# Kernel optimization log

Measured on AMD Instinct MI355X. Metric: run time of the kernel, lower is better.

Reference implementation:

```python
import jax, jax.numpy as jnp
import numpy as np
import string

N_QUBITS = 16
N_LAYERS = 2
BATCH = 32
DIM = 2 ** N_QUBITS


def _apply_1q(psi, U, q):
    # psi: (B,) + (2,)*n complex; U: (2,2) complex acting on qubit q
    n = psi.ndim - 1
    ax = string.ascii_lowercase[:n]
    out = list(ax)
    out[q] = 'A'
    return jnp.einsum('A' + ax[q] + ',z' + ax + '->z' + ''.join(out), U, psi)


def _apply_2q(psi, G, c, t):
    # G: (2,2,2,2) = (out_c, out_t, in_c, in_t)
    n = psi.ndim - 1
    ax = string.ascii_lowercase[:n]
    out = list(ax)
    out[c] = 'A'
    out[t] = 'B'
    return jnp.einsum('AB' + ax[c] + ax[t] + ',z' + ax + '->z' + ''.join(out), G, psi)


def _rx(th):
    c = jnp.cos(th * 0.5).astype(jnp.complex64)
    s = jnp.sin(th * 0.5).astype(jnp.complex64)
    return jnp.array([[c, -1j * s], [-1j * s, c]])


def _ry(th):
    c = jnp.cos(th * 0.5).astype(jnp.complex64)
    s = jnp.sin(th * 0.5).astype(jnp.complex64)
    return jnp.array([[c, -s], [s, c]])


def _rz(th):
    th_c = th.astype(jnp.complex64)
    z = jnp.zeros((), jnp.complex64)
    return jnp.array([[jnp.exp(-0.5j * th_c), z], [z, jnp.exp(0.5j * th_c)]])


_CNOT = jnp.array([[1, 0, 0, 0],
                   [0, 1, 0, 0],
                   [0, 0, 0, 1],
                   [0, 0, 1, 0]], dtype=jnp.complex64).reshape(2, 2, 2, 2)


def setup_inputs() -> dict:
    key = jax.random.key(0)
    k1, k2, k3 = jax.random.split(key, 3)
    thetas = jax.random.normal(k1, (N_LAYERS, 3, N_QUBITS), dtype=jnp.float32)
    re = jax.random.normal(k2, (BATCH, DIM), dtype=jnp.float32)
    im = jax.random.normal(k3, (BATCH, DIM), dtype=jnp.float32)
    norm = jnp.sqrt(jnp.sum(re * re + im * im, axis=-1, keepdims=True))
    return {"thetas": thetas, "state_re": re / norm, "state_im": im / norm}


def reference(thetas, state_re, state_im):
    B = state_re.shape[0]
    psi = (state_re.astype(jnp.complex64) + 1j * state_im.astype(jnp.complex64))
    psi = psi.reshape((B,) + (2,) * N_QUBITS)
    for l in range(N_LAYERS):
        for q in range(N_QUBITS):
            psi = _apply_1q(psi, _rx(thetas[l, 0, q]), q)
            psi = _apply_1q(psi, _ry(thetas[l, 1, q]), q)
            psi = _apply_1q(psi, _rz(thetas[l, 2, q]), q)
        for q in range(N_QUBITS):
            psi = _apply_2q(psi, _CNOT, q, (q + 1) % N_QUBITS)
    probs = (psi.real ** 2 + psi.imag ** 2).reshape(B, -1)
    return probs
```

## Files before the change

### kernel.cpp

```cpp
#include <hip/hip_runtime.h>


#define NT 256

__device__ __forceinline__ int fperm(int x) {
  int y = x ^ (x >> 1);
  y ^= (x & 1) ? 0xC000 : 0;
  return y & 0xFFFF;
}

__device__ __forceinline__ int finv16(int x) {
  int s = x;
  s ^= s >> 1; s ^= s >> 2; s ^= s >> 4; s ^= s >> 8;
  int b15 = ((s ^ (s >> 15)) & 1) << 15;
  return (s & 0x7FFF) | b15;
}

__device__ __forceinline__ int swz1(int l) { return l ^ ((l >> 4) & 31); }
__device__ __forceinline__ int swz2(int l) { return l ^ ((l >> 5) & 31); }

__device__ __forceinline__ void compute_gates(const float* __restrict__ th, float* gsh) {
  int tid = threadIdx.x;
  if (tid < 32) {
    int l = tid >> 4, q = tid & 15;
    float tx = th[l * 48 + q], ty = th[l * 48 + 16 + q], tz = th[l * 48 + 32 + q];
    float cx, sx, cy, sy, cz, sz;
    sincosf(0.5f * tx, &sx, &cx);
    sincosf(0.5f * ty, &sy, &cy);
    sincosf(0.5f * tz, &sz, &cz);
    float m00r = cy * cx, m00i =  sy * sx;
    float m01r = -sy * cx, m01i = -cy * sx;
    float m10r =  sy * cx, m10i = -cy * sx;
    float m11r =  cy * cx, m11i = -sy * sx;
    float* G = gsh + tid * 8;
    G[0] = cz * m00r + sz * m00i;  G[1] = cz * m00i - sz * m00r;
    G[2] = cz * m01r + sz * m01i;  G[3] = cz * m01i - sz * m01r;
    G[4] = cz * m10r - sz * m10i;  G[5] = cz * m10i + sz * m10r;
    G[6] = cz * m11r - sz * m11i;  G[7] = cz * m11i + sz * m11r;
  }
}

template <int MK, int SK, int N>
__device__ __forceinline__ void greg(float (&ar)[N], float (&ai)[N],
                                     const float* G, int c) {
  const float4* G4 = (const float4*)G;
  float4 r0 = G4[0], r1 = G4[1];
  bool sw = (c != 0);
  float h00r = sw ? r1.z : r0.x, h00i = sw ? r1.w : r0.y;
  float h01r = sw ? r1.x : r0.z, h01i = sw ? r1.y : r0.w;
  float h10r = sw ? r0.z : r1.x, h10i = sw ? r0.w : r1.y;
  float h11r = sw ? r0.x : r1.z, h11i = sw ? r0.y : r1.w;
  constexpr int PV = MK & (-MK);
#pragma unroll
  for (int k = 0; k < N; k++) {
    if (k & PV) continue;
    const int k2 = k ^ MK;
    const int p0 = __builtin_popcount(k & SK) & 1;
    const int ka = p0 ? k2 : k;
    const int kb = p0 ? k : k2;
    float xr = ar[ka], xi = ai[ka], yr = ar[kb], yi = ai[kb];
    ar[ka] = h00r * xr - h00i * xi + h01r * yr - h01i * yi;
    ai[ka] = h00r * xi + h00i * xr + h01r * yi + h01i * yr;
    ar[kb] = h10r * xr - h10i * xi + h11r * yr - h11i * yi;
    ai[kb] = h10r * xi + h10i * xr + h11r * yi + h11i * yr;
  }
}

__global__ void __launch_bounds__(NT) pass1_k(const float* __restrict__ th,
                                              const float* __restrict__ xre,
                                              const float* __restrict__ xim,
                                              float2* __restrict__ ws) {
  __shared__ float gsh[256];
  __shared__ float sre[4096], sim[4096];
  int t = threadIdx.x;
  int blk = blockIdx.x, batch = blk >> 4, wb = blk & 15;
  int base = batch * 65536 + (wb << 12);
  float ar[16], ai[16];

  compute_gates(th, gsh);
  {
    const float4* xr4 = (const float4*)(xre + base + (t << 4));
    const float4* xi4 = (const float4*)(xim + base + (t << 4));
#pragma unroll
    for (int q = 0; q < 4; q++) {
      float4 v = xr4[q]; ar[4*q] = v.x; ar[4*q+1] = v.y; ar[4*q+2] = v.z; ar[4*q+3] = v.w;
      float4 w = xi4[q]; ai[4*q] = w.x; ai[4*q+1] = w.y; ai[4*q+2] = w.z; ai[4*q+3] = w.w;
    }
  }
  __syncthreads();
  greg<1, 1>(ar, ai, gsh + 15 * 8, 0);
  greg<2, 2>(ar, ai, gsh + 14 * 8, 0);
  greg<4, 4>(ar, ai, gsh + 13 * 8, 0);
  greg<8, 8>(ar, ai, gsh + 12 * 8, 0);
#pragma unroll
  for (int k = 0; k < 16; k++) { int s = swz1((t << 4) | k); sre[s] = ar[k]; sim[s] = ai[k]; }
  __syncthreads();
#pragma unroll
  for (int k = 0; k < 16; k++) {
    int s = swz1((t & 15) | (k << 4) | ((t >> 4) << 8));
    ar[k] = sre[s]; ai[k] = sim[s];
  }
  greg<1, 1>(ar, ai, gsh + 11 * 8, 0);
  greg<2, 2>(ar, ai, gsh + 10 * 8, 0);
  greg<4, 4>(ar, ai, gsh + 9 * 8, 0);
  greg<8, 8>(ar, ai, gsh + 8 * 8, 0);
#pragma unroll
  for (int k = 0; k < 16; k++) {
    int s = swz1((t & 15) | (k << 4) | ((t >> 4) << 8));
    sre[s] = ar[k]; sim[s] = ai[k];
  }
  __syncthreads();
#pragma unroll
  for (int k = 0; k < 16; k++) {
    int s = swz1(t | (k << 8)); ar[k] = sre[s]; ai[k] = sim[s];
  }
  greg<1, 1>(ar, ai, gsh + 7 * 8, 0);
  greg<2, 2>(ar, ai, gsh + 6 * 8, 0);
  greg<4, 4>(ar, ai, gsh + 5 * 8, 0);
  greg<8, 8>(ar, ai, gsh + 4 * 8, 0);
#pragma unroll
  for (int k = 0; k < 16; k++)
    ws[base + t + (k << 8)] = make_float2(ar[k], ai[k]);
}

__global__ void __launch_bounds__(NT) pass2_k(const float* __restrict__ th,
                                              float2* __restrict__ ws) {
  __shared__ float gsh[256];
  __shared__ float sre[4096], sim[4096];
  int t = threadIdx.x;
  int blk = blockIdx.x, batch = blk >> 4, wb = blk & 15;
  int bbase = batch * 65536;
  float ar[16], ai[16];

  compute_gates(th, gsh);
#pragma unroll
  for (int k = 0; k < 16; k++) {
    float2 v = ws[bbase + t + (wb << 8) + (k << 12)];
    ar[k] = v.x; ai[k] = v.y;
  }
  __syncthreads();
  int cA = (__popc(t) + __popc(wb)) & 1;
  greg<1, 1>(ar, ai, gsh + 3 * 8, 0);
  greg<2, 2>(ar, ai, gsh + 2 * 8, 0);
  greg<4, 4>(ar, ai, gsh + 1 * 8, 0);
  greg<8, 8>(ar, ai, gsh + 0 * 8, 0);
  greg<12, 7>(ar, ai, gsh + (16 + 0) * 8, cA);
  greg<6, 12>(ar, ai, gsh + (16 + 1) * 8, 0);
  greg<3, 14>(ar, ai, gsh + (16 + 2) * 8, 0);
#pragma unroll
  for (int k = 0; k < 16; k++) {
    int s = swz2(t | (k << 8)); sre[s] = ar[k]; sim[s] = ai[k];
  }
  __syncthreads();
#pragma unroll
  for (int k = 0; k < 16; k++) {
    int s = swz2((k & 3) | (t << 2) | ((k >> 2) << 10));
    ar[k] = sre[s]; ai[k] = sim[s];
  }
  greg<13, 15>(ar, ai, gsh + (16 + 15) * 8, cA);
  greg<3, 14>(ar, ai, gsh + (16 + 14) * 8, cA);
#pragma unroll
  for (int k = 0; k < 16; k++) {
    int s = swz2((k & 3) | (t << 2) | ((k >> 2) << 10));
    sre[s] = ar[k]; sim[s] = ai[k];
  }
  __syncthreads();
#pragma unroll
  for (int k = 0; k < 16; k++) {
    int s = swz2((t & 1) | (k << 1) | ((t >> 1) << 5));
    ar[k] = sre[s]; ai[k] = sim[s];
  }
  {
    int cC = (__popc(t >> 1) + __popc(wb)) & 1;
    greg<3, 14>(ar, ai, gsh + (16 + 13) * 8, cC);
    greg<6, 12>(ar, ai, gsh + (16 + 12) * 8, cC);
    greg<12, 8>(ar, ai, gsh + (16 + 11) * 8, cC);
  }
#pragma unroll
  for (int k = 0; k < 16; k++) {
    int s = swz2((t & 1) | (k << 1) | ((t >> 1) << 5));
    sre[s] = ar[k]; sim[s] = ai[k];
  }
  __syncthreads();
#pragma unroll
  for (int k = 0; k < 16; k++) {
    int s = swz2((t & 15) | (k << 4) | ((t >> 4) << 8));
    ar[k] = sre[s]; ai[k] = sim[s];
  }
  {
    int cD = (__popc(t >> 4) + __popc(wb)) & 1;
    greg<3, 14>(ar, ai, gsh + (16 + 10) * 8, cD);
    greg<6, 12>(ar, ai, gsh + (16 + 9) * 8, cD);
    greg<12, 8>(ar, ai, gsh + (16 + 8) * 8, cD);
  }
#pragma unroll
  for (int k = 0; k < 16; k++) {
    int full = (t & 15) | (k << 4) | (wb << 8) | ((t >> 4) << 12);
    ws[bbase + full] = make_float2(ar[k], ai[k]);
  }
}

__global__ void __launch_bounds__(NT) pass3_k(const float* __restrict__ th,
                                              const float2* __restrict__ ws,
                                              float* __restrict__ out) {
  __shared__ float gsh[256];
  int t = threadIdx.x;
  int blk = blockIdx.x, batch = blk >> 3, g3 = blk & 7;
  int bbase = batch * 65536;
  int jt = t | (g3 << 13);
  float ar[32], ai[32];
  compute_gates(th, gsh);
#pragma unroll
  for (int k = 0; k < 32; k++) {
    int j = jt | (k << 8);
    float2 v = ws[bbase + fperm(j)];
    ar[k] = v.x; ai[k] = v.y;
  }
  __syncthreads();
  greg<1, 1>(ar, ai, gsh + (16 + 7) * 8, 0);
  greg<2, 2>(ar, ai, gsh + (16 + 6) * 8, 0);
  greg<4, 4>(ar, ai, gsh + (16 + 5) * 8, 0);
  greg<8, 8>(ar, ai, gsh + (16 + 4) * 8, 0);
  greg<16, 16>(ar, ai, gsh + (16 + 3) * 8, 0);
#pragma unroll
  for (int k = 0; k < 32; k++) {
    int j = jt | (k << 8);
    out[bbase + finv16(j)] = ar[k] * ar[k] + ai[k] * ai[k];
  }
}

extern "C" void kernel_launch(void* const* d_in, const int* in_sizes, int n_in,
                              void* d_out, int out_size, void* d_ws, size_t ws_size,
                              hipStream_t stream) {
  const float* th  = (const float*)d_in[0];
  const float* xre = (const float*)d_in[1];
  const float* xim = (const float*)d_in[2];
  float* out = (float*)d_out;

  float2* amp = (float2*)d_ws;

  pass1_k<<<512, NT, 0, stream>>>(th, xre, xim, amp);
  pass2_k<<<512, NT, 0, stream>>>(th, amp);
  pass3_k<<<256, NT, 0, stream>>>(th, amp, out);
}
```

Baseline: 104.2 us.

## Fuse three passes into one cooperative kernel with per-batch atomic counters

Merges the three separate kernel launches into a single cooperative kernel. The phases are synchronized per batch with global atomic counters and spin-waits instead of kernel boundaries, which lets batches progress independently and removes the launch gaps between passes. It adds a memset, an occupancy query and fence/atomic overhead on every call. It relies on co-residency of all 512 blocks and falls back to the three-kernel path if the cooperative launch fails.

```diff
diff --git a/kernel.cpp b/kernel.cpp
--- a/kernel.cpp
+++ b/kernel.cpp
@@ -66,6 +66,155 @@
   }
 }
 
+
+__device__ __forceinline__ void phaseA_body(int t, int bbase, int wb,
+                                            const float* gsh,
+                                            float* sre, float* sim,
+                                            const float* __restrict__ xre,
+                                            const float* __restrict__ xim,
+                                            float2* __restrict__ ws) {
+  float ar[16], ai[16];
+  int base = bbase + (wb << 12);
+  const float4* xr4 = (const float4*)(xre + base + (t << 4));
+  const float4* xi4 = (const float4*)(xim + base + (t << 4));
+#pragma unroll
+  for (int q = 0; q < 4; q++) {
+    float4 v = xr4[q]; ar[4*q] = v.x; ar[4*q+1] = v.y; ar[4*q+2] = v.z; ar[4*q+3] = v.w;
+    float4 w = xi4[q]; ai[4*q] = w.x; ai[4*q+1] = w.y; ai[4*q+2] = w.z; ai[4*q+3] = w.w;
+  }
+  __syncthreads();
+  greg<1, 1>(ar, ai, gsh + 15 * 8, 0);
+  greg<2, 2>(ar, ai, gsh + 14 * 8, 0);
+  greg<4, 4>(ar, ai, gsh + 13 * 8, 0);
+  greg<8, 8>(ar, ai, gsh + 12 * 8, 0);
+#pragma unroll
+  for (int k = 0; k < 16; k++) { int s = swz1((t << 4) | k); sre[s] = ar[k]; sim[s] = ai[k]; }
+  __syncthreads();
+#pragma unroll
+  for (int k = 0; k < 16; k++) {
+    int s = swz1((t & 15) | (k << 4) | ((t >> 4) << 8));
+    ar[k] = sre[s]; ai[k] = sim[s];
+  }
+  greg<1, 1>(ar, ai, gsh + 11 * 8, 0);
+  greg<2, 2>(ar, ai, gsh + 10 * 8, 0);
+  greg<4, 4>(ar, ai, gsh + 9 * 8, 0);
+  greg<8, 8>(ar, ai, gsh + 8 * 8, 0);
+#pragma unroll
+  for (int k = 0; k < 16; k++) {
+    int s = swz1((t & 15) | (k << 4) | ((t >> 4) << 8));
+    sre[s] = ar[k]; sim[s] = ai[k];
+  }
+  __syncthreads();
+#pragma unroll
+  for (int k = 0; k < 16; k++) {
+    int s = swz1(t | (k << 8)); ar[k] = sre[s]; ai[k] = sim[s];
+  }
+  greg<1, 1>(ar, ai, gsh + 7 * 8, 0);
+  greg<2, 2>(ar, ai, gsh + 6 * 8, 0);
+  greg<4, 4>(ar, ai, gsh + 5 * 8, 0);
+  greg<8, 8>(ar, ai, gsh + 4 * 8, 0);
+#pragma unroll
+  for (int k = 0; k < 16; k++)
+    ws[base + t + (k << 8)] = make_float2(ar[k], ai[k]);
+}
+
+__device__ __forceinline__ void phaseB_body(int t, int bbase, int wb,
+                                            const float* gsh,
+                                            float* sre, float* sim,
+                                            float2* __restrict__ ws) {
+  float ar[16], ai[16];
+#pragma unroll
+  for (int k = 0; k < 16; k++) {
+    float2 v = ws[bbase + t + (wb << 8) + (k << 12)];
+    ar[k] = v.x; ai[k] = v.y;
+  }
+  int cA = (__popc(t) + __popc(wb)) & 1;
+  greg<1, 1>(ar, ai, gsh + 3 * 8, 0);
+  greg<2, 2>(ar, ai, gsh + 2 * 8, 0);
+  greg<4, 4>(ar, ai, gsh + 1 * 8, 0);
+  greg<8, 8>(ar, ai, gsh + 0 * 8, 0);
+  greg<12, 7>(ar, ai, gsh + (16 + 0) * 8, cA);
+  greg<6, 12>(ar, ai, gsh + (16 + 1) * 8, 0);
+  greg<3, 14>(ar, ai, gsh + (16 + 2) * 8, 0);
+  __syncthreads();
+#pragma unroll
+  for (int k = 0; k < 16; k++) {
+    int s = swz2(t | (k << 8)); sre[s] = ar[k]; sim[s] = ai[k];
+  }
+  __syncthreads();
+#pragma unroll
+  for (int k = 0; k < 16; k++) {
+    int s = swz2((k & 3) | (t << 2) | ((k >> 2) << 10));
+    ar[k] = sre[s]; ai[k] = sim[s];
+  }
+  greg<13, 15>(ar, ai, gsh + (16 + 15) * 8, cA);
+  greg<3, 14>(ar, ai, gsh + (16 + 14) * 8, cA);
+#pragma unroll
+  for (int k = 0; k < 16; k++) {
+    int s = swz2((k & 3) | (t << 2) | ((k >> 2) << 10));
+    sre[s] = ar[k]; sim[s] = ai[k];
+  }
+  __syncthreads();
+#pragma unroll
+  for (int k = 0; k < 16; k++) {
+    int s = swz2((t & 1) | (k << 1) | ((t >> 1) << 5));
+    ar[k] = sre[s]; ai[k] = sim[s];
+  }
+  {
+    int cC = (__popc(t >> 1) + __popc(wb)) & 1;
+    greg<3, 14>(ar, ai, gsh + (16 + 13) * 8, cC);
+    greg<6, 12>(ar, ai, gsh + (16 + 12) * 8, cC);
+    greg<12, 8>(ar, ai, gsh + (16 + 11) * 8, cC);
+  }
+#pragma unroll
+  for (int k = 0; k < 16; k++) {
+    int s = swz2((t & 1) | (k << 1) | ((t >> 1) << 5));
+    sre[s] = ar[k]; sim[s] = ai[k];
+  }
+  __syncthreads();
+#pragma unroll
+  for (int k = 0; k < 16; k++) {
+    int s = swz2((t & 15) | (k << 4) | ((t >> 4) << 8));
+    ar[k] = sre[s]; ai[k] = sim[s];
+  }
+  {
+    int cD = (__popc(t >> 4) + __popc(wb)) & 1;
+    greg<3, 14>(ar, ai, gsh + (16 + 10) * 8, cD);
+    greg<6, 12>(ar, ai, gsh + (16 + 9) * 8, cD);
+    greg<12, 8>(ar, ai, gsh + (16 + 8) * 8, cD);
+  }
+#pragma unroll
+  for (int k = 0; k < 16; k++) {
+    int full = (t & 15) | (k << 4) | (wb << 8) | ((t >> 4) << 12);
+    ws[bbase + full] = make_float2(ar[k], ai[k]);
+  }
+}
+
+__device__ __forceinline__ void phaseC_body(int t, int bbase3, int g3,
+                                            const float* gsh,
+                                            const float2* __restrict__ ws,
+                                            float* __restrict__ out) {
+  int jt = t | (g3 << 13);
+  float br[32], bi[32];
+#pragma unroll
+  for (int k = 0; k < 32; k++) {
+    int j = jt | (k << 8);
+    float2 v = ws[bbase3 + fperm(j)];
+    br[k] = v.x; bi[k] = v.y;
+  }
+  greg<1, 1>(br, bi, gsh + (16 + 7) * 8, 0);
+  greg<2, 2>(br, bi, gsh + (16 + 6) * 8, 0);
+  greg<4, 4>(br, bi, gsh + (16 + 5) * 8, 0);
+  greg<8, 8>(br, bi, gsh + (16 + 4) * 8, 0);
+  greg<16, 16>(br, bi, gsh + (16 + 3) * 8, 0);
+#pragma unroll
+  for (int k = 0; k < 32; k++) {
+    int j = jt | (k << 8);
+    out[bbase3 + finv16(j)] = br[k] * br[k] + bi[k] * bi[k];
+  }
+}
+
+
 __global__ void __launch_bounds__(NT) pass1_k(const float* __restrict__ th,
                                               const float* __restrict__ xre,
                                               const float* __restrict__ xim,
@@ -74,53 +223,8 @@
   __shared__ float sre[4096], sim[4096];
   int t = threadIdx.x;
   int blk = blockIdx.x, batch = blk >> 4, wb = blk & 15;
-  int base = batch * 65536 + (wb << 12);
-  float ar[16], ai[16];
-
   compute_gates(th, gsh);
-  {
-    const float4* xr4 = (const float4*)(xre + base + (t << 4));
-    const float4* xi4 = (const float4*)(xim + base + (t << 4));
-#pragma unroll
-    for (int q = 0; q < 4; q++) {
-      float4 v = xr4[q]; ar[4*q] = v.x; ar[4*q+1] = v.y; ar[4*q+2] = v.z; ar[4*q+3] = v.w;
-      float4 w = xi4[q]; ai[4*q] = w.x; ai[4*q+1] = w.y; ai[4*q+2] = w.z; ai[4*q+3] = w.w;
-    }
-  }
-  __syncthreads();
-  greg<1, 1>(ar, ai, gsh + 15 * 8, 0);
-  greg<2, 2>(ar, ai, gsh + 14 * 8, 0);
-  greg<4, 4>(ar, ai, gsh + 13 * 8, 0);
-  greg<8, 8>(ar, ai, gsh + 12 * 8, 0);
-#pragma unroll
-  for (int k = 0; k < 16; k++) { int s = swz1((t << 4) | k); sre[s] = ar[k]; sim[s] = ai[k]; }
-  __syncthreads();
-#pragma unroll
-  for (int k = 0; k < 16; k++) {
-    int s = swz1((t & 15) | (k << 4) | ((t >> 4) << 8));
-    ar[k] = sre[s]; ai[k] = sim[s];
-  }
-  greg<1, 1>(ar, ai, gsh + 11 * 8, 0);
-  greg<2, 2>(ar, ai, gsh + 10 * 8, 0);
-  greg<4, 4>(ar, ai, gsh + 9 * 8, 0);
-  greg<8, 8>(ar, ai, gsh + 8 * 8, 0);
-#pragma unroll
-  for (int k = 0; k < 16; k++) {
-    int s = swz1((t & 15) | (k << 4) | ((t >> 4) << 8));
-    sre[s] = ar[k]; sim[s] = ai[k];
-  }
-  __syncthreads();
-#pragma unroll
-  for (int k = 0; k < 16; k++) {
-    int s = swz1(t | (k << 8)); ar[k] = sre[s]; ai[k] = sim[s];
-  }
-  greg<1, 1>(ar, ai, gsh + 7 * 8, 0);
-  greg<2, 2>(ar, ai, gsh + 6 * 8, 0);
-  greg<4, 4>(ar, ai, gsh + 5 * 8, 0);
-  greg<8, 8>(ar, ai, gsh + 4 * 8, 0);
-#pragma unroll
-  for (int k = 0; k < 16; k++)
-    ws[base + t + (k << 8)] = make_float2(ar[k], ai[k]);
+  phaseA_body(t, batch * 65536, wb, gsh, sre, sim, xre, xim, ws);
 }
 
 __global__ void __launch_bounds__(NT) pass2_k(const float* __restrict__ th,
@@ -129,75 +233,9 @@
   __shared__ float sre[4096], sim[4096];
   int t = threadIdx.x;
   int blk = blockIdx.x, batch = blk >> 4, wb = blk & 15;
-  int bbase = batch * 65536;
-  float ar[16], ai[16];
-
   compute_gates(th, gsh);
-#pragma unroll
-  for (int k = 0; k < 16; k++) {
-    float2 v = ws[bbase + t + (wb << 8) + (k << 12)];
-    ar[k] = v.x; ai[k] = v.y;
-  }
-  __syncthreads();
-  int cA = (__popc(t) + __popc(wb)) & 1;
-  greg<1, 1>(ar, ai, gsh + 3 * 8, 0);
-  greg<2, 2>(ar, ai, gsh + 2 * 8, 0);
-  greg<4, 4>(ar, ai, gsh + 1 * 8, 0);
-  greg<8, 8>(ar, ai, gsh + 0 * 8, 0);
-  greg<12, 7>(ar, ai, gsh + (16 + 0) * 8, cA);
-  greg<6, 12>(ar, ai, gsh + (16 + 1) * 8, 0);
-  greg<3, 14>(ar, ai, gsh + (16 + 2) * 8, 0);
-#pragma unroll
-  for (int k = 0; k < 16; k++) {
-    int s = swz2(t | (k << 8)); sre[s] = ar[k]; sim[s] = ai[k];
-  }
-  __syncthreads();
-#pragma unroll
-  for (int k = 0; k < 16; k++) {
-    int s = swz2((k & 3) | (t << 2) | ((k >> 2) << 10));
-    ar[k] = sre[s]; ai[k] = sim[s];
-  }
-  greg<13, 15>(ar, ai, gsh + (16 + 15) * 8, cA);
-  greg<3, 14>(ar, ai, gsh + (16 + 14) * 8, cA);
-#pragma unroll
-  for (int k = 0; k < 16; k++) {
-    int s = swz2((k & 3) | (t << 2) | ((k >> 2) << 10));
-    sre[s] = ar[k]; sim[s] = ai[k];
-  }
-  __syncthreads();
-#pragma unroll
-  for (int k = 0; k < 16; k++) {
-    int s = swz2((t & 1) | (k << 1) | ((t >> 1) << 5));
-    ar[k] = sre[s]; ai[k] = sim[s];
-  }
-  {
-    int cC = (__popc(t >> 1) + __popc(wb)) & 1;
-    greg<3, 14>(ar, ai, gsh + (16 + 13) * 8, cC);
-    greg<6, 12>(ar, ai, gsh + (16 + 12) * 8, cC);
-    greg<12, 8>(ar, ai, gsh + (16 + 11) * 8, cC);
-  }
-#pragma unroll
-  for (int k = 0; k < 16; k++) {
-    int s = swz2((t & 1) | (k << 1) | ((t >> 1) << 5));
-    sre[s] = ar[k]; sim[s] = ai[k];
-  }
-  __syncthreads();
-#pragma unroll
-  for (int k = 0; k < 16; k++) {
-    int s = swz2((t & 15) | (k << 4) | ((t >> 4) << 8));
-    ar[k] = sre[s]; ai[k] = sim[s];
-  }
-  {
-    int cD = (__popc(t >> 4) + __popc(wb)) & 1;
-    greg<3, 14>(ar, ai, gsh + (16 + 10) * 8, cD);
-    greg<6, 12>(ar, ai, gsh + (16 + 9) * 8, cD);
-    greg<12, 8>(ar, ai, gsh + (16 + 8) * 8, cD);
-  }
-#pragma unroll
-  for (int k = 0; k < 16; k++) {
-    int full = (t & 15) | (k << 4) | (wb << 8) | ((t >> 4) << 12);
-    ws[bbase + full] = make_float2(ar[k], ai[k]);
-  }
+  __syncthreads();
+  phaseB_body(t, batch * 65536, wb, gsh, sre, sim, ws);
 }
 
 __global__ void __launch_bounds__(NT) pass3_k(const float* __restrict__ th,
@@ -206,28 +244,54 @@
   __shared__ float gsh[256];
   int t = threadIdx.x;
   int blk = blockIdx.x, batch = blk >> 3, g3 = blk & 7;
+  compute_gates(th, gsh);
+  __syncthreads();
+  phaseC_body(t, batch * 65536, g3, gsh, ws, out);
+}
+
+
+__device__ __forceinline__ void signal(unsigned* cnt) {
+  __threadfence();
+  __syncthreads();
+  if (threadIdx.x == 0)
+    __hip_atomic_fetch_add(cnt, 1u, __ATOMIC_RELEASE, __HIP_MEMORY_SCOPE_AGENT);
+}
+
+__device__ __forceinline__ void wait16(unsigned* cnt) {
+  if (threadIdx.x == 0) {
+    while (__hip_atomic_load(cnt, __ATOMIC_ACQUIRE, __HIP_MEMORY_SCOPE_AGENT) < 16u)
+      __builtin_amdgcn_s_sleep(1);
+  }
+  __syncthreads();
+  __threadfence();
+}
+
+__global__ void __launch_bounds__(NT, 2)
+fused_k(const float* __restrict__ th,
+        const float* __restrict__ xre, const float* __restrict__ xim,
+        float2* __restrict__ ws, float* __restrict__ out,
+        unsigned* __restrict__ cnt1, unsigned* __restrict__ cnt2) {
+  __shared__ float gsh[256];
+  __shared__ float sre[4096], sim[4096];
+  int t = threadIdx.x;
+  int blk = blockIdx.x;
+  int batch = blk >> 4, wb = blk & 15;
   int bbase = batch * 65536;
-  int jt = t | (g3 << 13);
-  float ar[32], ai[32];
+
   compute_gates(th, gsh);
-#pragma unroll
-  for (int k = 0; k < 32; k++) {
-    int j = jt | (k << 8);
-    float2 v = ws[bbase + fperm(j)];
-    ar[k] = v.x; ai[k] = v.y;
-  }
-  __syncthreads();
-  greg<1, 1>(ar, ai, gsh + (16 + 7) * 8, 0);
-  greg<2, 2>(ar, ai, gsh + (16 + 6) * 8, 0);
-  greg<4, 4>(ar, ai, gsh + (16 + 5) * 8, 0);
-  greg<8, 8>(ar, ai, gsh + (16 + 4) * 8, 0);
-  greg<16, 16>(ar, ai, gsh + (16 + 3) * 8, 0);
-#pragma unroll
-  for (int k = 0; k < 32; k++) {
-    int j = jt | (k << 8);
-    out[bbase + finv16(j)] = ar[k] * ar[k] + ai[k] * ai[k];
-  }
-}
+  phaseA_body(t, bbase, wb, gsh, sre, sim, xre, xim, ws);
+  signal(&cnt1[batch]);
+
+  wait16(&cnt1[batch]);
+  phaseB_body(t, bbase, wb, gsh, sre, sim, ws);
+  signal(&cnt2[batch]);
+
+  if (blk >= 256) return;
+  int batch3 = blk >> 3, g3 = blk & 7;
+  wait16(&cnt2[batch3]);
+  phaseC_body(t, batch3 * 65536, g3, gsh, ws, out);
+}
+
 
 extern "C" void kernel_launch(void* const* d_in, const int* in_sizes, int n_in,
                               void* d_out, int out_size, void* d_ws, size_t ws_size,
@@ -238,8 +302,27 @@
   float* out = (float*)d_out;
 
   float2* amp = (float2*)d_ws;
-
-  pass1_k<<<512, NT, 0, stream>>>(th, xre, xim, amp);
-  pass2_k<<<512, NT, 0, stream>>>(th, amp);
-  pass3_k<<<256, NT, 0, stream>>>(th, amp, out);
-}
+  unsigned* cnt1 = (unsigned*)((char*)d_ws + (16u << 20));
+  unsigned* cnt2 = cnt1 + 32;
+
+  int maxBlk = 0;
+  hipError_t qrc = hipOccupancyMaxActiveBlocksPerMultiprocessor(
+      &maxBlk, (const void*)fused_k, NT, 0);
+  bool try_coop = (qrc == hipSuccess && maxBlk >= 2);
+
+  bool coop_ok = false;
+  if (try_coop) {
+    hipMemsetAsync((void*)cnt1, 0, 64 * sizeof(unsigned), stream);
+    void* args[] = {(void*)&th, (void*)&xre, (void*)&xim,
+                    (void*)&amp, (void*)&out, (void*)&cnt1, (void*)&cnt2};
+    hipError_t rc = hipLaunchCooperativeKernel((const void*)fused_k, dim3(512),
+                                               dim3(NT), args, 0, stream);
+    coop_ok = (rc == hipSuccess);
+  }
+
+  if (!coop_ok) {
+    pass1_k<<<512, NT, 0, stream>>>(th, xre, xim, amp);
+    pass2_k<<<512, NT, 0, stream>>>(th, amp);
+    pass3_k<<<256, NT, 0, stream>>>(th, amp, out);
+  }
+}
```

Result: no change. 104.0 us (-0.1%).
